# Kernel optimization log

Hardware: AMD Instinct MI355X
Metric: run time of the kernel (lower is better)

## Reference

```python
import jax, jax.numpy as jnp
import numpy as np

BINS = 10
NUM_CLASSES = 2
BATCH = 8388608


def setup_inputs() -> dict:
    key = jax.random.key(0)
    k1, k2 = jax.random.split(key)
    x = jax.random.normal(k1, (BATCH, NUM_CLASSES), dtype=jnp.float32)
    target = jax.random.randint(k2, (BATCH,), 0, NUM_CLASSES).astype(jnp.int64)
    return {"x": x, "target": target}


def reference(x, target):
    # One-hot targets: y.scatter_(1, target, 1)
    y = jax.nn.one_hot(target, NUM_CLASSES, dtype=x.dtype)  # [B, C]

    # g = |d BCE / d logits| = |sigmoid(x) - y|, detached
    g = jax.lax.stop_gradient(jnp.abs(jax.nn.sigmoid(x) - y))

    # bin_idx = floor(g * (bins - 0.0001)); g in [0,1] -> idx in [0, bins-1]
    bin_idx = jnp.floor(g * (BINS - 0.0001)).astype(jnp.int32)  # [B, C]

    # Single-pass histogram instead of the per-bin Python loop
    bin_count = jnp.zeros((BINS,), dtype=x.dtype).at[bin_idx.reshape(-1)].add(1.0)

    N = x.shape[0] * x.shape[1]
    nonempty = jnp.sum(bin_count > 0).astype(x.dtype)
    gd = jnp.maximum(bin_count * nonempty, 0.0001)
    beta = N / gd  # [bins]

    weight = jax.lax.stop_gradient(beta[bin_idx])  # [B, C], constant wrt x

    # Stable BCE-with-logits, elementwise, then weighted mean (torch semantics)
    bce = jnp.maximum(x, 0.0) - x * y + jnp.log1p(jnp.exp(-jnp.abs(x)))
    return jnp.mean(weight * bce)
```

## Files before the change

### kernel.cpp

```cpp
#include <hip/hip_runtime.h>
#include <math.h>

#define BINS 10

constexpr int   NPAIRS = 4194304;
constexpr float NTOT_F = 16777216.0f;

constexpr int G1     = 2048;
constexpr int BLK    = 256;
constexpr int STRIDE = G1 * BLK;
constexpr int ITERS  = NPAIRS / STRIDE;

constexpr size_t WS_PAIR = 0;

struct alignas(8) Pair { float s; unsigned c; };

__device__ __forceinline__ void proc(float x, bool y1,
                                     float* __restrict__ acc,
                                     unsigned long long& cnt64) {
    float z = y1 ? -x : x;
    float t = __builtin_amdgcn_exp2f(z * 1.4426950408889634f);
    float u = 1.0f + t;
    float g = t * __builtin_amdgcn_rcpf(u);
    int   b = (int)(g * 9.9999f);
    b = b < 9 ? b : 9;
    float l = __builtin_amdgcn_logf(u);
    cnt64 += 1ull << (6 * b);
#pragma unroll
    for (int i = 0; i < BINS; ++i)
        acc[i] += (b == i) ? l : 0.0f;
}

__global__ __launch_bounds__(BLK) void ghm_main(const float4* __restrict__ x4,
                                                const int2*   __restrict__ t2,
                                                Pair*         __restrict__ blk_pair) {
    const int tid  = threadIdx.x;
    const int lane = tid & 63;
    const int wave = tid >> 6;

    float acc[BINS];
#pragma unroll
    for (int b = 0; b < BINS; ++b) acc[b] = 0.0f;
    unsigned long long cnt64 = 0ull;

    const int base = blockIdx.x * BLK + tid;
#pragma unroll
    for (int k = 0; k < ITERS; ++k) {
        float4 xv = x4[base + k * STRIDE];
        int2   tv = t2[base + k * STRIDE];
        proc(xv.x, tv.x == 0, acc, cnt64);
        proc(xv.y, tv.x == 1, acc, cnt64);
        proc(xv.z, tv.y == 0, acc, cnt64);
        proc(xv.w, tv.y == 1, acc, cnt64);
    }

    unsigned cnt[BINS];
#pragma unroll
    for (int b = 0; b < BINS; ++b) cnt[b] = (unsigned)((cnt64 >> (6 * b)) & 63ull);
#pragma unroll
    for (int b = 0; b < BINS; ++b) {
        for (int off = 32; off > 0; off >>= 1) {
            acc[b] += __shfl_down(acc[b], off, 64);
            cnt[b] += __shfl_down(cnt[b], off, 64);
        }
    }

    __shared__ Pair red[4][BINS];
    if (lane == 0) {
#pragma unroll
        for (int b = 0; b < BINS; ++b) red[wave][b] = Pair{acc[b], cnt[b]};
    }
    __syncthreads();
    if (tid < BINS) {
        float    s = red[0][tid].s + red[1][tid].s + red[2][tid].s + red[3][tid].s;
        unsigned c = red[0][tid].c + red[1][tid].c + red[2][tid].c + red[3][tid].c;
        blk_pair[tid * G1 + blockIdx.x] = Pair{s, c};
    }
}

__global__ __launch_bounds__(640) void ghm_final(const Pair* __restrict__ blk_pair,
                                                 float*      __restrict__ out) {
    const int wave = threadIdx.x >> 6;
    const int lane = threadIdx.x & 63;
    double s = 0.0, c = 0.0;
#pragma unroll
    for (int k = 0; k < G1 / 64; ++k) {
        Pair p = blk_pair[wave * G1 + k * 64 + lane];
        s += (double)p.s;
        c += (double)p.c;
    }
    for (int off = 32; off > 0; off >>= 1) {
        s += __shfl_down(s, off, 64);
        c += __shfl_down(c, off, 64);
    }
    __shared__ double Sb[BINS], Cb[BINS];
    if (lane == 0) { Sb[wave] = s; Cb[wave] = c; }
    __syncthreads();
    if (threadIdx.x == 0) {
        float nonempty = 0.0f;
#pragma unroll
        for (int b = 0; b < BINS; ++b) nonempty += (Cb[b] > 0.0) ? 1.0f : 0.0f;
        double tot = 0.0;
#pragma unroll
        for (int b = 0; b < BINS; ++b) {
            float gd   = fmaxf((float)Cb[b] * nonempty, 0.0001f);
            float beta = NTOT_F / gd;
            tot += (double)beta * Sb[b];
        }
        out[0] = (float)(tot * 0.693147180559945309 / (double)NTOT_F);
    }
}

extern "C" void kernel_launch(void* const* d_in, const int* in_sizes, int n_in,
                              void* d_out, int out_size, void* d_ws, size_t ws_size,
                              hipStream_t stream) {
    const float4* x4 = (const float4*)d_in[0];
    const int2*   t2 = (const int2*)d_in[1];

    Pair*  blk_pair = (Pair*)((char*)d_ws + WS_PAIR);
    float* out      = (float*)d_out;

    ghm_main <<<G1, BLK, 0, stream>>>(x4, t2, blk_pair);
    ghm_final<<<1, 640, 0, stream>>>(blk_pair, out);
}
```

Before: 120.7 us.

## Count bins with wave ballots and derive last bin from totals

Replaces the packed 64-bit per-thread bin counter with per-wave ballot/popcount counts for nine bins, and drops the per-thread accumulator for the last bin. The last bin's sum and count are recovered in the final kernel by subtracting the other bins from a total-loss sum and from the known element count. The block reduction moves from ten serial shuffle chains per wave into shared memory, with each wave reducing a subset of bins. This removes 64-bit shift/add work and some shuffle latency, but adds nine ballots per element and a subtraction in float and double that may lose precision for bin 9.

```diff
diff --git a/kernel.cpp b/kernel.cpp
--- a/kernel.cpp
+++ b/kernel.cpp
@@ -16,8 +16,8 @@
 struct alignas(8) Pair { float s; unsigned c; };
 
 __device__ __forceinline__ void proc(float x, bool y1,
-                                     float* __restrict__ acc,
-                                     unsigned long long& cnt64) {
+                                     float* __restrict__ acc, float& sumL,
+                                     unsigned* __restrict__ cw) {
     float z = y1 ? -x : x;
     float t = __builtin_amdgcn_exp2f(z * 1.4426950408889634f);
     float u = 1.0f + t;
@@ -25,10 +25,13 @@
     int   b = (int)(g * 9.9999f);
     b = b < 9 ? b : 9;
     float l = __builtin_amdgcn_logf(u);
-    cnt64 += 1ull << (6 * b);
+    sumL += l;
 #pragma unroll
-    for (int i = 0; i < BINS; ++i)
-        acc[i] += (b == i) ? l : 0.0f;
+    for (int i = 0; i < BINS - 1; ++i) {
+        bool hit = (b == i);
+        acc[i] += hit ? l : 0.0f;
+        cw[i]  += (unsigned)__popcll(__ballot(hit));
+    }
 }
 
 __global__ __launch_bounds__(BLK) void ghm_main(const float4* __restrict__ x4,
@@ -38,43 +41,45 @@
     const int lane = tid & 63;
     const int wave = tid >> 6;
 
-    float acc[BINS];
+    float acc[BINS - 1];
 #pragma unroll
-    for (int b = 0; b < BINS; ++b) acc[b] = 0.0f;
-    unsigned long long cnt64 = 0ull;
+    for (int b = 0; b < BINS - 1; ++b) acc[b] = 0.0f;
+    float sumL = 0.0f;
+    unsigned cw[BINS - 1];
+#pragma unroll
+    for (int b = 0; b < BINS - 1; ++b) cw[b] = 0u;
 
     const int base = blockIdx.x * BLK + tid;
 #pragma unroll
     for (int k = 0; k < ITERS; ++k) {
         float4 xv = x4[base + k * STRIDE];
         int2   tv = t2[base + k * STRIDE];
-        proc(xv.x, tv.x == 0, acc, cnt64);
-        proc(xv.y, tv.x == 1, acc, cnt64);
-        proc(xv.z, tv.y == 0, acc, cnt64);
-        proc(xv.w, tv.y == 1, acc, cnt64);
+        proc(xv.x, tv.x == 0, acc, sumL, cw);
+        proc(xv.y, tv.x == 1, acc, sumL, cw);
+        proc(xv.z, tv.y == 0, acc, sumL, cw);
+        proc(xv.w, tv.y == 1, acc, sumL, cw);
     }
 
-    unsigned cnt[BINS];
+    __shared__ float    lsum[BINS * BLK];
+    __shared__ unsigned lcnt[4][BINS - 1];
 #pragma unroll
-    for (int b = 0; b < BINS; ++b) cnt[b] = (unsigned)((cnt64 >> (6 * b)) & 63ull);
-#pragma unroll
-    for (int b = 0; b < BINS; ++b) {
-        for (int off = 32; off > 0; off >>= 1) {
-            acc[b] += __shfl_down(acc[b], off, 64);
-            cnt[b] += __shfl_down(cnt[b], off, 64);
-        }
-    }
-
-    __shared__ Pair red[4][BINS];
+    for (int b = 0; b < BINS - 1; ++b) lsum[b * BLK + tid] = acc[b];
+    lsum[9 * BLK + tid] = sumL;
     if (lane == 0) {
 #pragma unroll
-        for (int b = 0; b < BINS; ++b) red[wave][b] = Pair{acc[b], cnt[b]};
+        for (int b = 0; b < BINS - 1; ++b) lcnt[wave][b] = cw[b];
     }
     __syncthreads();
-    if (tid < BINS) {
-        float    s = red[0][tid].s + red[1][tid].s + red[2][tid].s + red[3][tid].s;
-        unsigned c = red[0][tid].c + red[1][tid].c + red[2][tid].c + red[3][tid].c;
-        blk_pair[tid * G1 + blockIdx.x] = Pair{s, c};
+
+    for (int b = wave; b < BINS; b += 4) {
+        float s = lsum[b * BLK + lane]       + lsum[b * BLK + lane + 64]
+                + lsum[b * BLK + lane + 128] + lsum[b * BLK + lane + 192];
+        for (int off = 32; off > 0; off >>= 1) s += __shfl_down(s, off, 64);
+        if (lane == 0) {
+            unsigned c = 0u;
+            if (b < BINS - 1) c = lcnt[0][b] + lcnt[1][b] + lcnt[2][b] + lcnt[3][b];
+            blk_pair[b * G1 + blockIdx.x] = Pair{s, c};
+        }
     }
 }
 
@@ -97,6 +102,10 @@
     if (lane == 0) { Sb[wave] = s; Cb[wave] = c; }
     __syncthreads();
     if (threadIdx.x == 0) {
+        double s9 = Sb[9], c9 = (double)NTOT_F;
+#pragma unroll
+        for (int b = 0; b < BINS - 1; ++b) { s9 -= Sb[b]; c9 -= Cb[b]; }
+        Sb[9] = s9; Cb[9] = c9;
         float nonempty = 0.0f;
 #pragma unroll
         for (int b = 0; b < BINS; ++b) nonempty += (Cb[b] > 0.0) ? 1.0f : 0.0f;
```

Measured after the change: 131.1 us. 8.6% more time.

## Fuse final reduction into main kernel via last-block ticket and derive bin 9

Applied to the files above, without the earlier changes.

Merges the two-kernel reduction into a single kernel. The last block to finish, detected with an atomic ticket, performs the global reduction. The per-bin shuffle reductions are replaced by a shared-memory column transpose followed by one shuffle tree per slot. Bin 9's sum and count are now derived from the total sum and element count, which removes one accumulator per element. In exchange it adds a memset launch, a threadfence and atomic per block, and the derived float subtraction may cost some precision.

```diff
diff --git a/kernel.cpp b/kernel.cpp
--- a/kernel.cpp
+++ b/kernel.cpp
@@ -11,12 +11,13 @@
 constexpr int STRIDE = G1 * BLK;
 constexpr int ITERS  = NPAIRS / STRIDE;
 
-constexpr size_t WS_PAIR = 0;
+constexpr int SLOTS = 19;
 
-struct alignas(8) Pair { float s; unsigned c; };
+constexpr size_t WS_ARR    = 0;
+constexpr size_t WS_TICKET = 160000;
 
 __device__ __forceinline__ void proc(float x, bool y1,
-                                     float* __restrict__ acc,
+                                     float* __restrict__ acc, float& sumL,
                                      unsigned long long& cnt64) {
     float z = y1 ? -x : x;
     float t = __builtin_amdgcn_exp2f(z * 1.4426950408889634f);
@@ -25,22 +26,26 @@
     int   b = (int)(g * 9.9999f);
     b = b < 9 ? b : 9;
     float l = __builtin_amdgcn_logf(u);
+    sumL += l;
     cnt64 += 1ull << (6 * b);
 #pragma unroll
-    for (int i = 0; i < BINS; ++i)
+    for (int i = 0; i < BINS - 1; ++i)
         acc[i] += (b == i) ? l : 0.0f;
 }
 
-__global__ __launch_bounds__(BLK) void ghm_main(const float4* __restrict__ x4,
-                                                const int2*   __restrict__ t2,
-                                                Pair*         __restrict__ blk_pair) {
+__global__ __launch_bounds__(BLK) void ghm_fused(const float4* __restrict__ x4,
+                                                 const int2*   __restrict__ t2,
+                                                 float*        __restrict__ arr,
+                                                 unsigned*     __restrict__ ticket,
+                                                 float*        __restrict__ out) {
     const int tid  = threadIdx.x;
     const int lane = tid & 63;
     const int wave = tid >> 6;
 
-    float acc[BINS];
+    float acc[BINS - 1];
 #pragma unroll
-    for (int b = 0; b < BINS; ++b) acc[b] = 0.0f;
+    for (int b = 0; b < BINS - 1; ++b) acc[b] = 0.0f;
+    float sumL = 0.0f;
     unsigned long long cnt64 = 0ull;
 
     const int base = blockIdx.x * BLK + tid;
@@ -48,55 +53,57 @@
     for (int k = 0; k < ITERS; ++k) {
         float4 xv = x4[base + k * STRIDE];
         int2   tv = t2[base + k * STRIDE];
-        proc(xv.x, tv.x == 0, acc, cnt64);
-        proc(xv.y, tv.x == 1, acc, cnt64);
-        proc(xv.z, tv.y == 0, acc, cnt64);
-        proc(xv.w, tv.y == 1, acc, cnt64);
+        proc(xv.x, tv.x == 0, acc, sumL, cnt64);
+        proc(xv.y, tv.x == 1, acc, sumL, cnt64);
+        proc(xv.z, tv.y == 0, acc, sumL, cnt64);
+        proc(xv.w, tv.y == 1, acc, sumL, cnt64);
     }
 
-    unsigned cnt[BINS];
+    __shared__ float cols[SLOTS * BLK];
 #pragma unroll
-    for (int b = 0; b < BINS; ++b) cnt[b] = (unsigned)((cnt64 >> (6 * b)) & 63ull);
+    for (int b = 0; b < BINS - 1; ++b) cols[b * BLK + tid] = acc[b];
+    cols[9 * BLK + tid] = sumL;
 #pragma unroll
-    for (int b = 0; b < BINS; ++b) {
-        for (int off = 32; off > 0; off >>= 1) {
-            acc[b] += __shfl_down(acc[b], off, 64);
-            cnt[b] += __shfl_down(cnt[b], off, 64);
-        }
+    for (int b = 0; b < BINS - 1; ++b)
+        cols[(10 + b) * BLK + tid] = (float)((cnt64 >> (6 * b)) & 63ull);
+    __syncthreads();
+
+    for (int s = wave; s < SLOTS; s += 4) {
+        float v = cols[s * BLK + lane]       + cols[s * BLK + lane + 64]
+                + cols[s * BLK + lane + 128] + cols[s * BLK + lane + 192];
+        for (int off = 32; off > 0; off >>= 1) v += __shfl_down(v, off, 64);
+        if (lane == 0) arr[s * G1 + blockIdx.x] = v;
     }
 
-    __shared__ Pair red[4][BINS];
-    if (lane == 0) {
-#pragma unroll
-        for (int b = 0; b < BINS; ++b) red[wave][b] = Pair{acc[b], cnt[b]};
+    __shared__ int amLast;
+    __syncthreads();
+    __threadfence();
+    if (tid == 0) {
+        unsigned old = atomicAdd(ticket, 1u);
+        amLast = (old == (unsigned)(G1 - 1)) ? 1 : 0;
     }
     __syncthreads();
-    if (tid < BINS) {
-        float    s = red[0][tid].s + red[1][tid].s + red[2][tid].s + red[3][tid].s;
-        unsigned c = red[0][tid].c + red[1][tid].c + red[2][tid].c + red[3][tid].c;
-        blk_pair[tid * G1 + blockIdx.x] = Pair{s, c};
+    if (!amLast) return;
+    __threadfence();
+
+    __shared__ double Red[SLOTS];
+    for (int s = wave; s < SLOTS; s += 4) {
+        double v = 0.0;
+#pragma unroll
+        for (int k = 0; k < G1 / 64; ++k) v += (double)arr[s * G1 + k * 64 + lane];
+        for (int off = 32; off > 0; off >>= 1) v += __shfl_down(v, off, 64);
+        if (lane == 0) Red[s] = v;
     }
-}
-
-__global__ __launch_bounds__(640) void ghm_final(const Pair* __restrict__ blk_pair,
-                                                 float*      __restrict__ out) {
-    const int wave = threadIdx.x >> 6;
-    const int lane = threadIdx.x & 63;
-    double s = 0.0, c = 0.0;
+    __syncthreads();
+    if (tid == 0) {
+        double Sb[BINS], Cb[BINS];
+        double s9 = Red[9], c9 = (double)NTOT_F;
 #pragma unroll
-    for (int k = 0; k < G1 / 64; ++k) {
-        Pair p = blk_pair[wave * G1 + k * 64 + lane];
-        s += (double)p.s;
-        c += (double)p.c;
-    }
-    for (int off = 32; off > 0; off >>= 1) {
-        s += __shfl_down(s, off, 64);
-        c += __shfl_down(c, off, 64);
-    }
-    __shared__ double Sb[BINS], Cb[BINS];
-    if (lane == 0) { Sb[wave] = s; Cb[wave] = c; }
-    __syncthreads();
-    if (threadIdx.x == 0) {
+        for (int b = 0; b < BINS - 1; ++b) {
+            Sb[b] = Red[b];      s9 -= Red[b];
+            Cb[b] = Red[10 + b]; c9 -= Red[10 + b];
+        }
+        Sb[9] = s9; Cb[9] = c9;
         float nonempty = 0.0f;
 #pragma unroll
         for (int b = 0; b < BINS; ++b) nonempty += (Cb[b] > 0.0) ? 1.0f : 0.0f;
@@ -117,9 +124,10 @@
     const float4* x4 = (const float4*)d_in[0];
     const int2*   t2 = (const int2*)d_in[1];
 
-    Pair*  blk_pair = (Pair*)((char*)d_ws + WS_PAIR);
-    float* out      = (float*)d_out;
+    float*    arr    = (float*)   ((char*)d_ws + WS_ARR);
+    unsigned* ticket = (unsigned*)((char*)d_ws + WS_TICKET);
+    float*    out    = (float*)d_out;
 
-    ghm_main <<<G1, BLK, 0, stream>>>(x4, t2, blk_pair);
-    ghm_final<<<1, 640, 0, stream>>>(blk_pair, out);
+    hipMemsetAsync(ticket, 0, sizeof(unsigned), stream);
+    ghm_fused<<<G1, BLK, 0, stream>>>(x4, t2, arr, ticket, out);
 }
```

Measured after the change: 387.8 us. 3.21x slower.
